# Kernel tuning notes

Hardware: AMD Instinct MI355X
Metric: run time of the kernel (lower is better)

The kernel has to match this reference:

```python
import jax, jax.numpy as jnp
import numpy as np
from jax import lax

ITERATIONS = 8
KT, KH, KW = 3, 7, 7


def _ssm_op(left, right):
    a1, b1 = left
    a2, b2 = right
    return (a1 * a2, a2 * b1 + b2)


def setup_inputs() -> dict:
    key = jax.random.key(0)
    k1, k2, k3 = jax.random.split(key, 3)
    B, T, H, W, C = 1, 16, 64, 64, 128
    x = jax.random.normal(k1, (B, T, H, W, C), dtype=jnp.float32)
    A_kernel = 0.02 * jax.random.normal(k2, (C, KT, KH, KW), dtype=jnp.float32)
    B_kernel = 0.02 * jax.random.normal(k3, (C, KT, KH, KW), dtype=jnp.float32)
    return {"x": x, "A_kernel": A_kernel, "B_kernel": B_kernel}


def _pad_kernel_fft(kern, T, H, W):
    # Place (C, kt, kh, kw) kernel circularly centered into a (C, T, H, W) canvas, FFT it.
    C = kern.shape[0]
    t_idx = (jnp.arange(KT) - KT // 2) % T
    h_idx = (jnp.arange(KH) - KH // 2) % H
    w_idx = (jnp.arange(KW) - KW // 2) % W
    tt, th, tw = jnp.meshgrid(t_idx, h_idx, w_idx, indexing="ij")
    padded = jnp.zeros((C, T, H, W), dtype=kern.dtype).at[:, tt, th, tw].set(kern)
    kf = jnp.fft.fftn(padded, axes=(1, 2, 3))  # (C, T, H, W) complex
    return kf.transpose(1, 2, 3, 0)[None, ...]  # (1, T, H, W, C)


def reference(x, A_kernel, B_kernel):
    B, T, H, W, C = x.shape
    A_stable = 0.9 * jnp.tanh(A_kernel)
    A_f = _pad_kernel_fft(A_stable, T, H, W)   # (1,T,H,W,C)
    B_f = _pad_kernel_fft(B_kernel, T, H, W)   # (1,T,H,W,C)
    x_f = jnp.fft.fftn(x, axes=(1, 2, 3))      # (B,T,H,W,C)
    Bx_f = B_f * x_f
    a_seq = jnp.broadcast_to(A_f, (ITERATIONS, B, T, H, W, C))
    b_seq = jnp.broadcast_to(Bx_f, (ITERATIONS, B, T, H, W, C))
    _, h_all_f = lax.associative_scan(_ssm_op, (a_seq, b_seq), axis=0)
    h_final = jnp.fft.ifftn(h_all_f[-1], axes=(1, 2, 3)).real
    return h_final
```

## Files before the change

### kernel.cpp

```cpp
#include <hip/hip_runtime.h>
#include <hip/hip_fp16.h>
#include <math.h>

#define TT 16
#define HH 64
#define WW 64
#define CC 128
#define PI2 6.283185307179586f

#define LROW(r) (((r) & 0x38) | ((((r) >> 3) ^ (r)) & 7))

__device__ __forceinline__ float2 cadd(float2 a, float2 b){ return make_float2(a.x+b.x, a.y+b.y); }
__device__ __forceinline__ float2 csub(float2 a, float2 b){ return make_float2(a.x-b.x, a.y-b.y); }
__device__ __forceinline__ float2 cmul(float2 a, float2 b) {
    return make_float2(a.x*b.x - a.y*b.y, a.x*b.y + a.y*b.x);
}
__device__ __forceinline__ float2 cmac(float2 acc, float2 a, float2 b) {
    acc.x = fmaf(a.x, b.x, fmaf(-a.y, b.y, acc.x));
    acc.y = fmaf(a.x, b.y, fmaf(a.y, b.x, acc.y));
    return acc;
}
__device__ __forceinline__ float2 csq(float2 a) {
    return make_float2(a.x*a.x - a.y*a.y, 2.f*a.x*a.y);
}

template<int SGN>
__device__ __forceinline__ void dft4(float2 b0, float2 b1, float2 b2, float2 b3,
                                     float2& y0, float2& y1, float2& y2, float2& y3) {
    float2 e0 = cadd(b0, b2), e1 = csub(b0, b2);
    float2 o0 = cadd(b1, b3), o1 = csub(b1, b3);
    y0 = cadd(e0, o0); y2 = csub(e0, o0);
    float2 r = make_float2((float)(-SGN) * o1.y, (float)SGN * o1.x);
    y1 = cadd(e1, r); y3 = csub(e1, r);
}

template<int SGN>
__device__ __forceinline__ void dft8(const float2* a, float2* X) {
    const float C = 0.70710678118654752f;
    float2 E0,E1,E2,E3,O0,O1,O2,O3;
    dft4<SGN>(a[0],a[2],a[4],a[6], E0,E1,E2,E3);
    dft4<SGN>(a[1],a[3],a[5],a[7], O0,O1,O2,O3);
    float2 T1 = make_float2(C*(O1.x - (float)SGN*O1.y), C*((float)SGN*O1.x + O1.y));
    float2 T2 = make_float2((float)(-SGN)*O2.y, (float)SGN*O2.x);
    float2 T3 = make_float2(-C*(O3.x + (float)SGN*O3.y), C*((float)SGN*O3.x - O3.y));
    X[0]=cadd(E0,O0); X[4]=csub(E0,O0);
    X[1]=cadd(E1,T1); X[5]=csub(E1,T1);
    X[2]=cadd(E2,T2); X[6]=csub(E2,T2);
    X[3]=cadd(E3,T3); X[7]=csub(E3,T3);
}

template<int SGN>
__device__ __forceinline__ void dft16(const float2* v, float2* X) {
    const float ct[10] = {1.f, 0.92387953251f, 0.70710678119f, 0.38268343236f, 0.f,
                          0.f, -0.70710678119f, 0.f, 0.f, -0.92387953251f};
    const float st[10] = {0.f, 0.38268343236f, 0.70710678119f, 0.92387953251f, 1.f,
                          0.f, 0.70710678119f, 0.f, 0.f, -0.38268343236f};
    float2 Z[16];
    #pragma unroll
    for (int h0 = 0; h0 < 4; ++h0) {
        float2 y0,y1,y2,y3;
        dft4<SGN>(v[h0], v[4+h0], v[8+h0], v[12+h0], y0,y1,y2,y3);
        float2 ys[4] = {y0,y1,y2,y3};
        #pragma unroll
        for (int k0 = 0; k0 < 4; ++k0) {
            int m = h0 * k0;
            float cc = ct[m], ss = (float)SGN * st[m];
            Z[k0*4 + h0] = make_float2(ys[k0].x*cc - ys[k0].y*ss,
                                       ys[k0].x*ss + ys[k0].y*cc);
        }
    }
    #pragma unroll
    for (int k0 = 0; k0 < 4; ++k0) {
        float2 y0,y1,y2,y3;
        dft4<SGN>(Z[k0*4+0], Z[k0*4+1], Z[k0*4+2], Z[k0*4+3], y0,y1,y2,y3);
        X[k0] = y0; X[k0+4] = y1; X[k0+8] = y2; X[k0+12] = y3;
    }
}


__global__ __launch_bounds__(256) void pA(const float* __restrict__ x,
                                          uint4* __restrict__ Z,
                                          const float* __restrict__ Ak,
                                          const float* __restrict__ Bk,
                                          __half2* __restrict__ Ahw,
                                          __half2* __restrict__ Bhw) {
    __shared__ __align__(16) char smem[33280];
    int bid = blockIdx.x;
    int tid = threadIdx.x;
    if (bid < 1024) {
        float (*rf)[32]        = (float(*)[32])smem;
        __half2 (*sp)[33][32]  = (__half2(*)[33][32])(smem + 8192);
        float2* tw64           = (float2*)(smem + 8192 + 16896);
        __half2* zal           = (__half2*)smem;
        int cq = bid & 3, hq = (bid >> 2) & 15, t = bid >> 6;
        if (tid < 64) {
            float s, cw; sincosf(-PI2 * tid / 64.0f, &s, &cw);
            tw64[tid] = make_float2(cw, s);
        }
        int c = tid & 31, s4 = tid >> 5;
        for (int hh = 0; hh < 4; ++hh) {
            const float4* src4 = (const float4*)(x + (size_t)(t*64 + hq*4 + hh) * 64 * 128);
            for (int i = tid; i < 512; i += 256) {
                int w = i >> 3, j = i & 7;
                float4 v = src4[w * 32 + cq * 8 + j];
                rf[w][j*4+0] = v.x; rf[w][j*4+1] = v.y;
                rf[w][j*4+2] = v.z; rf[w][j*4+3] = v.w;
            }
            __syncthreads();
            float ar[8];
            #pragma unroll
            for (int h1 = 0; h1 < 8; ++h1) ar[h1] = rf[h1*8 + s4][c];
            __syncthreads();
            {
                float2 a[8], Y[8];
                #pragma unroll
                for (int h1 = 0; h1 < 8; ++h1) a[h1] = make_float2(ar[h1], 0.f);
                dft8<-1>(a, Y);
                #pragma unroll
                for (int k0 = 0; k0 < 8; ++k0) {
                    float2 z = cmul(Y[k0], tw64[(s4 * k0) & 63]);
                    zal[(k0*8 + s4) * 32 + c] = __float22half2_rn(z);
                }
            }
            __syncthreads();
            {
                float2 b[8], X[8];
                #pragma unroll
                for (int h0 = 0; h0 < 8; ++h0)
                    b[h0] = __half22float2(zal[(s4*8 + h0) * 32 + c]);
                dft8<-1>(b, X);
                #pragma unroll
                for (int k1 = 0; k1 < 8; ++k1) {
                    int om = s4 + 8 * k1;
                    if (om <= 32) sp[hh][om][c] = __float22half2_rn(X[k1]);
                }
            }
            __syncthreads();
        }
        for (int i = tid; i < 1056; i += 256) {
            int hh = i & 3, ccl = (i >> 2) & 7, om = i >> 5;
            uint4 u = *(const uint4*)&sp[hh][om][ccl * 4];
            Z[(((size_t)(om*32 + cq*8 + ccl)*16 + t)*64 + hq*4 + hh)] = u;
        }
    } else {
        float (*Asl)[7][64] = (float(*)[7][64])smem;
        float (*Bsl)[7][64] = (float(*)[7][64])(smem + 12544);
        float2 (*Awl)[64]   = (float2(*)[64])(smem + 25088);
        float2 (*Bwl)[64]   = (float2(*)[64])(smem + 28672);
        float2* tw64        = (float2*)(smem + 32256);
        int kid = bid - 1024;
        int kt = kid / 66;
        int rem = kid % 66;
        int om = rem >> 1, chalf = rem & 1;
        int c0 = chalf * 64;
        for (int i = tid; i < 64; i += 256) {
            float s, cw; sincosf(-PI2 * i / 64.0f, &s, &cw);
            tw64[i] = make_float2(cw, s);
        }
        for (int i = tid; i < 49 * 64; i += 256) {
            int p = i >> 6, cl = i & 63;
            int kh = p / 7, kw = p % 7;
            int idx = (((c0 + cl) * 3 + kt) * 7 + kh) * 7 + kw;
            Asl[kh][kw][cl] = 0.9f * tanhf(Ak[idx]);
            Bsl[kh][kw][cl] = Bk[idx];
        }
        __syncthreads();
        for (int i = tid; i < 7 * 64; i += 256) {
            int kh = i >> 6, cl = i & 63;
            float2 aA = make_float2(0.f,0.f), aB = make_float2(0.f,0.f);
            #pragma unroll
            for (int kw = 0; kw < 7; ++kw) {
                float2 tw = tw64[(om * (kw - 3)) & 63];
                float va = Asl[kh][kw][cl], vb = Bsl[kh][kw][cl];
                aA.x = fmaf(va, tw.x, aA.x); aA.y = fmaf(va, tw.y, aA.y);
                aB.x = fmaf(vb, tw.x, aB.x); aB.y = fmaf(vb, tw.y, aB.y);
            }
            Awl[kh][cl] = aA; Bwl[kh][cl] = aB;
        }
        __syncthreads();
        for (int i = tid; i < 64 * 64; i += 256) {
            int eta = i >> 6, cl = i & 63;
            float2 aA = make_float2(0.f,0.f), aB = make_float2(0.f,0.f);
            #pragma unroll
            for (int kh = 0; kh < 7; ++kh) {
                float2 tw = tw64[(eta * (kh - 3)) & 63];
                aA = cmac(aA, Awl[kh][cl], tw);
                aB = cmac(aB, Bwl[kh][cl], tw);
            }
            int ep = ((eta & 7) << 3) | (eta >> 3);
            int o = ((kt * 33 + om) * 64 + ep) * 128 + c0 + cl;
            Ahw[o] = __float22half2_rn(aA);
            Bhw[o] = __float22half2_rn(aB);
        }
    }
}

__global__ __launch_bounds__(256) void pmid(uint4* __restrict__ Z,
                                            const __half2* __restrict__ Ahw,
                                            const __half2* __restrict__ Bhw) {
    __shared__ __half2 tl[16][64][4];
    int l = (blockIdx.x & 7) * 132 + (blockIdx.x >> 3);
    int om = l >> 5, cc = l & 31;
    int c0 = cc * 4;
    int tid = threadIdx.x;
    uint4* g = Z + (size_t)l * 1024;

    int d = tid & 7;
    float twc[8], tws[8];
    {
        float s1, c1; sincosf(-PI2 * d / 64.0f, &s1, &c1);
        twc[0] = 1.f; tws[0] = 0.f;
        #pragma unroll
        for (int k = 1; k < 8; ++k) {
            twc[k] = twc[k-1]*c1 - tws[k-1]*s1;
            tws[k] = twc[k-1]*s1 + tws[k-1]*c1;
        }
    }
    for (int i = tid; i < 1024; i += 256) {
        uint4 u = g[i];
        int t = i >> 6, h = i & 63;
        int pr = LROW(h);
        tl[t][pr][0] = *(__half2*)&u.x;
        tl[t][pr][1] = *(__half2*)&u.y;
        tl[t][pr][2] = *(__half2*)&u.z;
        tl[t][pr][3] = *(__half2*)&u.w;
    }
    __syncthreads();
    int cl = (tid >> 3) & 3, ts = tid >> 5;
    #pragma unroll
    for (int q = 0; q < 2; ++q) {
        int t = ts*2 + q;
        float2 a[8], Y[8];
        #pragma unroll
        for (int h1 = 0; h1 < 8; ++h1)
            a[h1] = __half22float2(tl[t][LROW(h1*8 + d)][cl]);
        dft8<-1>(a, Y);
        #pragma unroll
        for (int k0 = 0; k0 < 8; ++k0) {
            float2 z = make_float2(Y[k0].x*twc[k0] - Y[k0].y*tws[k0],
                                   Y[k0].x*tws[k0] + Y[k0].y*twc[k0]);
            tl[t][LROW(k0*8 + d)][cl] = __float22half2_rn(z);
        }
    }
    __syncthreads();
    #pragma unroll
    for (int q = 0; q < 2; ++q) {
        int t = ts*2 + q;
        float2 a[8], Y[8];
        #pragma unroll
        for (int h0 = 0; h0 < 8; ++h0)
            a[h0] = __half22float2(tl[t][LROW(d*8 + h0)][cl]);
        dft8<-1>(a, Y);
        #pragma unroll
        for (int k1 = 0; k1 < 8; ++k1)
            tl[t][LROW(d*8 + k1)][cl] = __float22half2_rn(Y[k1]);
    }
    __syncthreads();
    {
        const float CT16[16] = {1.f, 0.9238795325f, 0.7071067812f, 0.3826834324f, 0.f,
                                -0.3826834324f, -0.7071067812f, -0.9238795325f, -1.f,
                                -0.9238795325f, -0.7071067812f, -0.3826834324f, 0.f,
                                0.3826834324f, 0.7071067812f, 0.9238795325f};
        const float ST16[16] = {0.f, 0.3826834324f, 0.7071067812f, 0.9238795325f, 1.f,
                                0.9238795325f, 0.7071067812f, 0.3826834324f, 0.f,
                                -0.3826834324f, -0.7071067812f, -0.9238795325f, -1.f,
                                -0.9238795325f, -0.7071067812f, -0.3826834324f};
        int cg = tid & 3, rT = tid >> 2;
        const int PKT = 33 * 64 * 128;
        int kb = (om * 64 + rT) * 128 + c0 + cg;
        float2 A0 = __half22float2(Ahw[kb]);
        float2 A1 = __half22float2(Ahw[kb + PKT]);
        float2 A2 = __half22float2(Ahw[kb + 2*PKT]);
        float2 B0 = __half22float2(Bhw[kb]);
        float2 B1 = __half22float2(Bhw[kb + PKT]);
        float2 B2 = __half22float2(Bhw[kb + 2*PKT]);
        int pr = LROW(rT);
        float2 v[16], X[16];
        #pragma unroll
        for (int t = 0; t < 16; ++t) v[t] = __half22float2(tl[t][pr][cg]);
        dft16<-1>(v, X);
        #pragma unroll
        for (int ta = 0; ta < 16; ++ta) {
            float2 wv = make_float2(CT16[ta], -ST16[ta]);
            float2 wc = make_float2(CT16[ta],  ST16[ta]);
            float2 Af = A1; Af = cmac(Af, A0, wc); Af = cmac(Af, A2, wv);
            float2 Bf = B1; Bf = cmac(Bf, B0, wc); Bf = cmac(Bf, B2, wv);
            float2 A2q = csq(Af), A4q = csq(A2q);
            float2 S = cmul(make_float2(1.f+Af.x, Af.y), make_float2(1.f+A2q.x, A2q.y));
            S = cmul(S, make_float2(1.f+A4q.x, A4q.y));
            float2 G = cmul(S, Bf);
            X[ta] = cmul(X[ta], G);
        }
        dft16<1>(X, v);
        const float sc = 0.015625f;
        #pragma unroll
        for (int t = 0; t < 16; ++t)
            tl[t][pr][cg] = __float22half2_rn(make_float2(v[t].x*sc, v[t].y*sc));
    }
    __syncthreads();
    #pragma unroll
    for (int q = 0; q < 2; ++q) {
        int t = ts*2 + q;
        float2 a[8], Y[8];
        #pragma unroll
        for (int e1 = 0; e1 < 8; ++e1)
            a[e1] = __half22float2(tl[t][LROW(d*8 + e1)][cl]);
        dft8<1>(a, Y);
        #pragma unroll
        for (int h0 = 0; h0 < 8; ++h0) {
            float2 z = make_float2( Y[h0].x*twc[h0] + Y[h0].y*tws[h0],
                                   -Y[h0].x*tws[h0] + Y[h0].y*twc[h0]);
            tl[t][LROW(d*8 + h0)][cl] = __float22half2_rn(z);
        }
    }
    __syncthreads();
    #pragma unroll
    for (int q = 0; q < 2; ++q) {
        int t = ts*2 + q;
        float2 a[8], Y[8];
        #pragma unroll
        for (int e0 = 0; e0 < 8; ++e0)
            a[e0] = __half22float2(tl[t][LROW(e0*8 + d)][cl]);
        dft8<1>(a, Y);
        #pragma unroll
        for (int h1 = 0; h1 < 8; ++h1)
            tl[t][LROW(d + 8*h1)][cl] = __float22half2_rn(Y[h1]);
    }
    __syncthreads();
    for (int i = tid; i < 1024; i += 256) {
        int t = i >> 6, h = i & 63;
        int pr = LROW(h);
        uint4 u;
        __half2 v0 = tl[t][pr][0], v1 = tl[t][pr][1];
        __half2 v2 = tl[t][pr][2], v3 = tl[t][pr][3];
        u.x = *(unsigned int*)&v0; u.y = *(unsigned int*)&v1;
        u.z = *(unsigned int*)&v2; u.w = *(unsigned int*)&v3;
        g[i] = u;
    }
}

__global__ __launch_bounds__(256) void p5(const uint4* __restrict__ Z,
                                          float* __restrict__ out) {
    __shared__ __half2 sp[4][33][32];
    __shared__ __half2 plane[64][32];
    __shared__ float2 tw64[64];
    int bid = blockIdx.x;
    int cq = bid & 3, hq = (bid >> 2) & 15, t = bid >> 6;
    int tid = threadIdx.x;
    if (tid < 64) {
        float s, cw; sincosf(PI2 * tid / 64.0f, &s, &cw);
        tw64[tid] = make_float2(cw, s);
    }
    for (int i = tid; i < 1056; i += 256) {
        int hh = i & 3, ccl = (i >> 2) & 7, om = i >> 5;
        uint4 u = Z[(((size_t)(om*32 + cq*8 + ccl)*16 + t)*64 + hq*4 + hh)];
        *(uint4*)&sp[hh][om][ccl * 4] = u;
    }
    __syncthreads();
    int c = tid & 31, s4 = tid >> 5;
    for (int hh = 0; hh < 4; ++hh) {
        for (int i = tid; i < 1056; i += 256) {
            int om = i >> 5, cl = i & 31;
            __half2 v = sp[hh][om][cl];
            plane[om][cl] = v;
            if (om >= 1 && om <= 31) {
                __half2 m = v; m.y = __hneg(m.y);
                plane[64 - om][cl] = m;
            }
        }
        __syncthreads();
        float2 ar[8];
        #pragma unroll
        for (int h1 = 0; h1 < 8; ++h1)
            ar[h1] = __half22float2(plane[h1*8 + s4][c]);
        __syncthreads();
        {
            float2 Y[8];
            dft8<1>(ar, Y);
            #pragma unroll
            for (int k0 = 0; k0 < 8; ++k0) {
                float2 z = cmul(Y[k0], tw64[(s4 * k0) & 63]);
                plane[k0*8 + s4][c] = __float22half2_rn(z);
            }
        }
        __syncthreads();
        {
            float2 b[8], X[8];
            #pragma unroll
            for (int h0 = 0; h0 < 8; ++h0)
                b[h0] = __half22float2(plane[s4*8 + h0][c]);
            dft8<1>(b, X);
            float* dst = out + (size_t)(t*64 + hq*4 + hh) * 64 * 128 + cq * 32 + c;
            #pragma unroll
            for (int k1 = 0; k1 < 8; ++k1)
                dst[(size_t)(s4 + 8*k1) * 128] = X[k1].x * (1.0f / 1024.0f);
        }
        __syncthreads();
    }
}

extern "C" void kernel_launch(void* const* d_in, const int* in_sizes, int n_in,
                              void* d_out, int out_size, void* d_ws, size_t ws_size,
                              hipStream_t stream) {
    const float* x  = (const float*)d_in[0];
    const float* Ak = (const float*)d_in[1];
    const float* Bk = (const float*)d_in[2];
    float* out = (float*)d_out;

    uint4* Z = (uint4*)d_ws;
    __half2* Ahw = (__half2*)((char*)d_ws + (size_t)33*32*1024*16);
    __half2* Bhw = Ahw + 3 * 33 * 64 * 128;

    hipLaunchKernelGGL(pA,   dim3(1222), dim3(256), 0, stream, x, Z, Ak, Bk, Ahw, Bhw);
    hipLaunchKernelGGL(pmid, dim3(1056), dim3(256), 0, stream, Z, Ahw, Bhw);
    hipLaunchKernelGGL(p5,   dim3(1024), dim3(256), 0, stream, Z, out);
}
```

Before: 65.76 us.

## Batch four rows per phase in first and last FFT stages to cut barriers

In the forward W-FFT stage, x is now loaded straight from global into registers (strided per-thread loads instead of float4 through shared memory). All four rows are processed per phase with shared buffers sized for four planes, and twiddles come from a per-thread recurrence instead of a shared table. The inverse stage does the same: it expands the Hermitian conjugate half into four full planes at load time and runs each FFT pass over all four rows between barriers. This cuts the number of __syncthreads, but raises shared memory per block and register pressure, which may lower occupancy, and the new global loads are less coalesced.

```diff
diff --git a/kernel.cpp b/kernel.cpp
--- a/kernel.cpp
+++ b/kernel.cpp
@@ -84,59 +84,59 @@
                                           const float* __restrict__ Bk,
                                           __half2* __restrict__ Ahw,
                                           __half2* __restrict__ Bhw) {
-    __shared__ __align__(16) char smem[33280];
+    __shared__ __align__(16) char smem[49664];
     int bid = blockIdx.x;
     int tid = threadIdx.x;
     if (bid < 1024) {
-        float (*rf)[32]        = (float(*)[32])smem;
-        __half2 (*sp)[33][32]  = (__half2(*)[33][32])(smem + 8192);
-        float2* tw64           = (float2*)(smem + 8192 + 16896);
-        __half2* zal           = (__half2*)smem;
+        __half2 (*zs)[64][32] = (__half2(*)[64][32])smem;
+        __half2 (*sp)[33][32] = (__half2(*)[33][32])(smem + 32768);
         int cq = bid & 3, hq = (bid >> 2) & 15, t = bid >> 6;
-        if (tid < 64) {
-            float s, cw; sincosf(-PI2 * tid / 64.0f, &s, &cw);
-            tw64[tid] = make_float2(cw, s);
-        }
         int c = tid & 31, s4 = tid >> 5;
+        float twc[8], tws[8];
+        {
+            float s1, c1; sincosf(-PI2 * s4 / 64.0f, &s1, &c1);
+            twc[0] = 1.f; tws[0] = 0.f;
+            #pragma unroll
+            for (int k = 1; k < 8; ++k) {
+                twc[k] = twc[k-1]*c1 - tws[k-1]*s1;
+                tws[k] = twc[k-1]*s1 + tws[k-1]*c1;
+            }
+        }
+        const float* xb = x + (size_t)(t*64 + hq*4) * 8192 + cq * 32 + c;
+        float xr[4][8];
+        #pragma unroll
+        for (int hh = 0; hh < 4; ++hh)
+            #pragma unroll
+            for (int h1 = 0; h1 < 8; ++h1)
+                xr[hh][h1] = xb[(size_t)hh * 8192 + (h1*8 + s4) * 128];
+        #pragma unroll
         for (int hh = 0; hh < 4; ++hh) {
-            const float4* src4 = (const float4*)(x + (size_t)(t*64 + hq*4 + hh) * 64 * 128);
-            for (int i = tid; i < 512; i += 256) {
-                int w = i >> 3, j = i & 7;
-                float4 v = src4[w * 32 + cq * 8 + j];
-                rf[w][j*4+0] = v.x; rf[w][j*4+1] = v.y;
-                rf[w][j*4+2] = v.z; rf[w][j*4+3] = v.w;
+            float2 a[8], Y[8];
+            #pragma unroll
+            for (int h1 = 0; h1 < 8; ++h1) a[h1] = make_float2(xr[hh][h1], 0.f);
+            dft8<-1>(a, Y);
+            #pragma unroll
+            for (int k0 = 0; k0 < 8; ++k0) {
+                float2 z = make_float2(Y[k0].x*twc[k0] - Y[k0].y*tws[k0],
+                                       Y[k0].x*tws[k0] + Y[k0].y*twc[k0]);
+                zs[hh][k0*8 + s4][c] = __float22half2_rn(z);
             }
-            __syncthreads();
-            float ar[8];
-            #pragma unroll
-            for (int h1 = 0; h1 < 8; ++h1) ar[h1] = rf[h1*8 + s4][c];
-            __syncthreads();
-            {
-                float2 a[8], Y[8];
-                #pragma unroll
-                for (int h1 = 0; h1 < 8; ++h1) a[h1] = make_float2(ar[h1], 0.f);
-                dft8<-1>(a, Y);
-                #pragma unroll
-                for (int k0 = 0; k0 < 8; ++k0) {
-                    float2 z = cmul(Y[k0], tw64[(s4 * k0) & 63]);
-                    zal[(k0*8 + s4) * 32 + c] = __float22half2_rn(z);
-                }
+        }
+        __syncthreads();
+        #pragma unroll
+        for (int hh = 0; hh < 4; ++hh) {
+            float2 b[8], X[8];
+            #pragma unroll
+            for (int h0 = 0; h0 < 8; ++h0)
+                b[h0] = __half22float2(zs[hh][s4*8 + h0][c]);
+            dft8<-1>(b, X);
+            #pragma unroll
+            for (int k1 = 0; k1 < 8; ++k1) {
+                int om = s4 + 8 * k1;
+                if (om <= 32) sp[hh][om][c] = __float22half2_rn(X[k1]);
             }
-            __syncthreads();
-            {
-                float2 b[8], X[8];
-                #pragma unroll
-                for (int h0 = 0; h0 < 8; ++h0)
-                    b[h0] = __half22float2(zal[(s4*8 + h0) * 32 + c]);
-                dft8<-1>(b, X);
-                #pragma unroll
-                for (int k1 = 0; k1 < 8; ++k1) {
-                    int om = s4 + 8 * k1;
-                    if (om <= 32) sp[hh][om][c] = __float22half2_rn(X[k1]);
-                }
-            }
-            __syncthreads();
-        }
+        }
+        __syncthreads();
         for (int i = tid; i < 1056; i += 256) {
             int hh = i & 3, ccl = (i >> 2) & 7, om = i >> 5;
             uint4 u = *(const uint4*)&sp[hh][om][ccl * 4];
@@ -341,8 +341,7 @@
 
 __global__ __launch_bounds__(256) void p5(const uint4* __restrict__ Z,
                                           float* __restrict__ out) {
-    __shared__ __half2 sp[4][33][32];
-    __shared__ __half2 plane[64][32];
+    __shared__ __half2 plane[4][64][32];
     __shared__ float2 tw64[64];
     int bid = blockIdx.x;
     int cq = bid & 3, hq = (bid >> 2) & 15, t = bid >> 6;
@@ -354,48 +353,51 @@
     for (int i = tid; i < 1056; i += 256) {
         int hh = i & 3, ccl = (i >> 2) & 7, om = i >> 5;
         uint4 u = Z[(((size_t)(om*32 + cq*8 + ccl)*16 + t)*64 + hq*4 + hh)];
-        *(uint4*)&sp[hh][om][ccl * 4] = u;
+        *(uint4*)&plane[hh][om][ccl * 4] = u;
+        if (om >= 1 && om <= 31) {
+            __half2 m0 = *(__half2*)&u.x; m0.y = __hneg(m0.y);
+            __half2 m1 = *(__half2*)&u.y; m1.y = __hneg(m1.y);
+            __half2 m2 = *(__half2*)&u.z; m2.y = __hneg(m2.y);
+            __half2 m3 = *(__half2*)&u.w; m3.y = __hneg(m3.y);
+            plane[hh][64-om][ccl*4+0] = m0;
+            plane[hh][64-om][ccl*4+1] = m1;
+            plane[hh][64-om][ccl*4+2] = m2;
+            plane[hh][64-om][ccl*4+3] = m3;
+        }
     }
     __syncthreads();
     int c = tid & 31, s4 = tid >> 5;
+    __half2 arh[4][8];
+    #pragma unroll
+    for (int hh = 0; hh < 4; ++hh)
+        #pragma unroll
+        for (int h1 = 0; h1 < 8; ++h1)
+            arh[hh][h1] = plane[hh][h1*8 + s4][c];
+    __syncthreads();
+    #pragma unroll
     for (int hh = 0; hh < 4; ++hh) {
-        for (int i = tid; i < 1056; i += 256) {
-            int om = i >> 5, cl = i & 31;
-            __half2 v = sp[hh][om][cl];
-            plane[om][cl] = v;
-            if (om >= 1 && om <= 31) {
-                __half2 m = v; m.y = __hneg(m.y);
-                plane[64 - om][cl] = m;
-            }
-        }
-        __syncthreads();
-        float2 ar[8];
-        #pragma unroll
-        for (int h1 = 0; h1 < 8; ++h1)
-            ar[h1] = __half22float2(plane[h1*8 + s4][c]);
-        __syncthreads();
-        {
-            float2 Y[8];
-            dft8<1>(ar, Y);
-            #pragma unroll
-            for (int k0 = 0; k0 < 8; ++k0) {
-                float2 z = cmul(Y[k0], tw64[(s4 * k0) & 63]);
-                plane[k0*8 + s4][c] = __float22half2_rn(z);
-            }
-        }
-        __syncthreads();
-        {
-            float2 b[8], X[8];
-            #pragma unroll
-            for (int h0 = 0; h0 < 8; ++h0)
-                b[h0] = __half22float2(plane[s4*8 + h0][c]);
-            dft8<1>(b, X);
-            float* dst = out + (size_t)(t*64 + hq*4 + hh) * 64 * 128 + cq * 32 + c;
-            #pragma unroll
-            for (int k1 = 0; k1 < 8; ++k1)
-                dst[(size_t)(s4 + 8*k1) * 128] = X[k1].x * (1.0f / 1024.0f);
-        }
-        __syncthreads();
+        float2 a[8], Y[8];
+        #pragma unroll
+        for (int h1 = 0; h1 < 8; ++h1) a[h1] = __half22float2(arh[hh][h1]);
+        dft8<1>(a, Y);
+        #pragma unroll
+        for (int k0 = 0; k0 < 8; ++k0) {
+            float2 z = cmul(Y[k0], tw64[(s4 * k0) & 63]);
+            plane[hh][k0*8 + s4][c] = __float22half2_rn(z);
+        }
+    }
+    __syncthreads();
+    #pragma unroll
+    for (int hh = 0; hh < 4; ++hh) {
+        float2 b[8], X[8];
+        #pragma unroll
+        for (int h0 = 0; h0 < 8; ++h0)
+            b[h0] = __half22float2(plane[hh][s4*8 + h0][c]);
+        dft8<1>(b, X);
+        float* dst = out + (size_t)(t*64 + hq*4 + hh) * 64 * 128 + cq * 32 + c;
+        #pragma unroll
+        for (int k1 = 0; k1 < 8; ++k1)
+            dst[(size_t)(s4 + 8*k1) * 128] = X[k1].x * (1.0f / 1024.0f);
     }
 }
 
```

Result: faster. 63.84 us (-2.9%).
